# Performance work log

Measured on AMD Instinct MI355X. Metric: run time of the kernel, lower is better.

Reference implementation:

```python
import jax, jax.numpy as jnp
import numpy as np

N = 100000      # nodes
E = 1200000     # edges
F_IN = 256      # features_num
HID = 64        # hidden_dim = max(64, 2*32)
NC = 32         # num_class
H = 2           # GAT heads (edge_num < 1.4M)
GAT_SLOPE = 0.2 # GATConv internal LeakyReLU
ACT_SLOPE = 0.01  # F.leaky_relu default


def _glorot(k, shape):
    lim = float(np.sqrt(6.0 / (shape[0] + shape[-1])))
    return jax.random.uniform(k, shape, minval=-lim, maxval=lim, dtype=jnp.float32)


def setup_inputs() -> dict:
    key = jax.random.key(0)
    ks = jax.random.split(key, 32)
    inp = {
        "x": jax.random.normal(ks[0], (N, F_IN), dtype=jnp.float32),
        "edge_index": jax.random.randint(ks[1], (2, E), 0, N, dtype=jnp.int32),
        "edge_weight": jax.random.uniform(ks[2], (E,), dtype=jnp.float32),
    }
    in_dims = [F_IN, 3 * HID]  # layer2 input is cell.output_dim = HID*(1+H)
    ki = 3
    for l, d in enumerate(in_dims):
        inp[f"pre_W{l}"] = _glorot(ks[ki], (d, HID)); ki += 1
        inp[f"pre_b{l}"] = jnp.zeros((HID,), jnp.float32)
        inp[f"gat_W{l}"] = _glorot(ks[ki], (HID, H * HID)); ki += 1
        inp[f"att_src{l}"] = _glorot(ks[ki], (H, HID)); ki += 1
        inp[f"att_dst{l}"] = _glorot(ks[ki], (H, HID)); ki += 1
        inp[f"gat_b{l}"] = jnp.zeros((H * HID,), jnp.float32)
        inp[f"sg_W{l}"] = _glorot(ks[ki], (HID, HID)); ki += 1
        inp[f"sg_b{l}"] = jnp.zeros((HID,), jnp.float32)
    inp["cls_W"] = _glorot(ks[ki], (3 * HID, NC))
    inp["cls_b"] = jnp.zeros((NC,), jnp.float32)
    return inp


def _gat_conv(x, src, dst, W, att_src, att_dst, b):
    # src/dst already include self-loops. x: [N, HID]
    xp = (x @ W).reshape(N, H, HID)                       # [N, H, C]
    a_src = jnp.sum(xp * att_src, axis=-1)                # [N, H]
    a_dst = jnp.sum(xp * att_dst, axis=-1)                # [N, H]
    e = jax.nn.leaky_relu(a_src[src] + a_dst[dst], GAT_SLOPE)  # [E', H]
    m = jax.ops.segment_max(e, dst, num_segments=N)       # segment softmax over dst
    e = jnp.exp(e - m[dst])
    s = jax.ops.segment_sum(e, dst, num_segments=N)
    alpha = e / (s[dst] + 1e-16)
    out = jax.ops.segment_sum(xp[src] * alpha[:, :, None], dst, num_segments=N)
    return out.reshape(N, H * HID) + b


def _sg_conv(x, src_sl, dst_sl, w_sl, W, b):
    # gcn_norm with self-loops (weight 1) already appended; K=1 propagation then linear
    deg = jax.ops.segment_sum(w_sl, dst_sl, num_segments=N)
    dinv = jnp.where(deg > 0, jax.lax.rsqrt(deg), 0.0)
    norm = dinv[src_sl] * w_sl * dinv[dst_sl]             # [E']
    h = jax.ops.segment_sum(x[src_sl] * norm[:, None], dst_sl, num_segments=N)
    return h @ W + b


def _forward(x, edge_index, edge_weight, params):
    src, dst = edge_index[0], edge_index[1]
    loop = jnp.arange(N, dtype=src.dtype)
    src_sl = jnp.concatenate([src, loop])
    dst_sl = jnp.concatenate([dst, loop])
    w_sl = jnp.concatenate([edge_weight, jnp.ones((N,), edge_weight.dtype)])
    for l in range(2):
        pre_W, pre_b, gat_W, a_s, a_d, gat_b, sg_W, sg_b = params[l]
        xh = x @ pre_W + pre_b                            # preprocessor_x
        o1 = jax.nn.leaky_relu(_gat_conv(xh, src_sl, dst_sl, gat_W, a_s, a_d, gat_b), ACT_SLOPE)
        o2 = jax.nn.leaky_relu(_sg_conv(xh, src_sl, dst_sl, w_sl, sg_W, sg_b), ACT_SLOPE)
        x = jax.nn.relu(jnp.concatenate([o1, o2], axis=1))  # [N, 3*HID]
    cls_W, cls_b = params[2]
    logits = x @ cls_W + cls_b
    return jax.nn.log_softmax(logits, axis=-1)


def reference(x, edge_index, edge_weight,
              pre_W0, pre_b0, gat_W0, att_src0, att_dst0, gat_b0, sg_W0, sg_b0,
              pre_W1, pre_b1, gat_W1, att_src1, att_dst1, gat_b1, sg_W1, sg_b1,
              cls_W, cls_b):
    params = [
        (pre_W0, pre_b0, gat_W0, att_src0, att_dst0, gat_b0, sg_W0, sg_b0),
        (pre_W1, pre_b1, gat_W1, att_src1, att_dst1, gat_b1, sg_W1, sg_b1),
        (cls_W, cls_b),
    ]
    return _forward(x, edge_index, edge_weight, params)
```

## Files before the change

kernel.cpp:

```cpp
#include <hip/hip_runtime.h>
#include <hip/hip_fp16.h>
#include <math.h>

#define NN 100000
#define NE 1200000
#define FIN 256
#define NBLK 391
#define HB 4688

using half8   = __attribute__((ext_vector_type(8))) _Float16;
using floatx4 = __attribute__((ext_vector_type(4))) float;

__device__ __forceinline__ floatx4 mfma16(half8 a, half8 b, floatx4 c) {
    return __builtin_amdgcn_mfma_f32_16x16x32_f16(a, b, c, 0, 0, 0);
}

__global__ __launch_bounds__(256) void k_prep(const int* __restrict__ dst,
                                              const float* __restrict__ ew,
                                              unsigned long long* __restrict__ packed,
                                              int* __restrict__ ord,
                                              const float* __restrict__ W0,
                                              const float* __restrict__ W1,
                                              const float* __restrict__ Wg0,
                                              const float* __restrict__ Ws0,
                                              const float* __restrict__ Wg1,
                                              const float* __restrict__ Ws1,
                                              const float* __restrict__ Wc,
                                              const float* __restrict__ As0,
                                              const float* __restrict__ Ad0,
                                              const float* __restrict__ As1,
                                              const float* __restrict__ Ad1,
                                              __half* __restrict__ Wf,
                                              float* __restrict__ attf) {
    int bid = blockIdx.x;
    if (bid < HB) {
        int e = bid * 256 + threadIdx.x;
        if (e >= NE) return;
        int d = dst[e]; float w = ew[e];
        unsigned long long add = (1ULL << 48)
            + (unsigned long long)((double)w * 4294967296.0);
        unsigned long long old = atomicAdd(&packed[d], add);
        ord[e] = (int)(old >> 48);
        return;
    }
    int o = (bid - HB) * 256 + threadIdx.x;
    if (o >= 59904) return;
    if (o >= 59392) {
        int idx = o - 59392;
        int layer = idx >> 8, rem = idx & 255;
        int v = rem >> 6, c = rem & 63, h = v & 1;
        const float* Wg = layer ? Wg1 : Wg0;
        const float* av = (v < 2) ? (layer ? As1 : As0) : (layer ? Ad1 : Ad0);
        float s = 0.f;
        for (int jj = 0; jj < 64; ++jj)
            s = fmaf(Wg[c * 128 + h * 64 + jj], av[h * 64 + jj], s);
        attf[idx] = s;
        return;
    }
    int lo, NT, N; const float* Wg; const float* Wsg = nullptr;
    if (o < 16384)      { lo = o;         NT = 4;  N = 64; Wg = W0; }
    else if (o < 28672) { lo = o - 16384; NT = 4;  N = 64; Wg = W1; }
    else if (o < 40960) { lo = o - 28672; NT = 12; N = 0;  Wg = Wg0; Wsg = Ws0; }
    else if (o < 53248) { lo = o - 40960; NT = 12; N = 0;  Wg = Wg1; Wsg = Ws1; }
    else                { lo = o - 53248; NT = 2;  N = 32; Wg = Wc; }
    int j = lo & 7, n = (lo >> 3) & 15, q = (lo >> 7) & 3, rest = lo >> 9;
    int t = rest % NT, kc = rest / NT;
    int k = kc * 32 + q * 8 + j, col = t * 16 + n;
    float v;
    if (Wsg) v = (col < 128) ? Wg[(size_t)k * 128 + col] : Wsg[(size_t)k * 64 + (col - 128)];
    else     v = Wg[(size_t)k * N + col];
    Wf[o] = __float2half(v);
}

__global__ __launch_bounds__(256) void k_scanA(const unsigned long long* __restrict__ packed,
                                               int* __restrict__ row_ptr,
                                               int* __restrict__ bsum,
                                               float* __restrict__ asd) {
    __shared__ int tmp[256];
    int tid = threadIdx.x;
    int i = blockIdx.x * 256 + tid;
    int v = 0;
    if (i < NN) {
        unsigned long long p = packed[i];
        v = (int)(p >> 48);
        double deg = (double)(p & 0xFFFFFFFFFFFFULL) * (1.0 / 4294967296.0) + 1.0;
        asd[i * 4 + 2] = rsqrtf((float)deg);
    }
    tmp[tid] = v;
    __syncthreads();
    for (int off = 1; off < 256; off <<= 1) {
        int t = (tid >= off) ? tmp[tid - off] : 0;
        __syncthreads();
        tmp[tid] += t;
        __syncthreads();
    }
    if (i < NN) row_ptr[i] = tmp[tid] - v;
    if (tid == 255) bsum[blockIdx.x] = tmp[255];
}

__global__ __launch_bounds__(512) void k_scanB(int* __restrict__ bsum) {
    __shared__ int tmp[512];
    int tid = threadIdx.x;
    int v = (tid < NBLK) ? bsum[tid] : 0;
    tmp[tid] = v;
    __syncthreads();
    for (int off = 1; off < 512; off <<= 1) {
        int t = (tid >= off) ? tmp[tid - off] : 0;
        __syncthreads();
        tmp[tid] += t;
        __syncthreads();
    }
    if (tid < NBLK) bsum[tid] = tmp[tid] - v;
}

__global__ __launch_bounds__(256) void k_scanC(int* __restrict__ row_ptr,
                                               const int* __restrict__ bsum) {
    int i = blockIdx.x * 256 + threadIdx.x;
    if (i < NN) row_ptr[i] += bsum[i >> 8];
    if (i == 0) row_ptr[NN] = NE;
}

__global__ __launch_bounds__(256) void k_fill(const int* __restrict__ src,
                                              const int* __restrict__ dst,
                                              const float* __restrict__ ew,
                                              const int* __restrict__ row_ptr,
                                              const int* __restrict__ ord,
                                              int2* __restrict__ recs) {
    int e = blockIdx.x * 256 + threadIdx.x;
    if (e >= NE) return;
    int d = dst[e];
    int pos = row_ptr[d] + ord[e];
    int2 r; r.x = src[e]; r.y = __float_as_int(ew[e]);
    recs[pos] = r;
}

__device__ __forceinline__ void pre_epi(floatx4* acc, const float* b, const float* attf,
                                        float* asd, float* a_dst, __half* out,
                                        int rowb, int q, int n) {
    float vs0[4] = {0,0,0,0}, vs1[4] = {0,0,0,0};
    float vd0[4] = {0,0,0,0}, vd1[4] = {0,0,0,0};
    #pragma unroll
    for (int t = 0; t < 4; ++t) {
        float bb  = b[t * 16 + n];
        float ws0 = attf[t * 16 + n],       ws1 = attf[64 + t * 16 + n];
        float wd0 = attf[128 + t * 16 + n], wd1 = attf[192 + t * 16 + n];
        #pragma unroll
        for (int r = 0; r < 4; ++r) {
            float xv = acc[t][r] + bb;
            int row = rowb + q * 4 + r;
            if (row < NN) out[(size_t)row * 64 + t * 16 + n] = __float2half(xv);
            vs0[r] = fmaf(xv, ws0, vs0[r]);
            vs1[r] = fmaf(xv, ws1, vs1[r]);
            vd0[r] = fmaf(xv, wd0, vd0[r]);
            vd1[r] = fmaf(xv, wd1, vd1[r]);
        }
    }
    #pragma unroll
    for (int off = 1; off < 16; off <<= 1) {
        #pragma unroll
        for (int r = 0; r < 4; ++r) {
            vs0[r] += __shfl_xor(vs0[r], off);
            vs1[r] += __shfl_xor(vs1[r], off);
            vd0[r] += __shfl_xor(vd0[r], off);
            vd1[r] += __shfl_xor(vd1[r], off);
        }
    }
    if (n == 0) {
        #pragma unroll
        for (int r = 0; r < 4; ++r) {
            int row = rowb + q * 4 + r;
            if (row < NN) {
                *(float2*)&asd[row * 4] = make_float2(vs0[r], vs1[r]);
                *(float2*)&a_dst[row * 2] = make_float2(vd0[r], vd1[r]);
            }
        }
    }
}

template<int KK>
__global__ __launch_bounds__(256) void k_pre32(const float* __restrict__ A,
                                               const __half* __restrict__ Wf,
                                               const float* __restrict__ b,
                                               const float* __restrict__ attf,
                                               float* __restrict__ asd,
                                               float* __restrict__ a_dst,
                                               __half* __restrict__ out) {
    int lane = threadIdx.x & 63, wv = threadIdx.x >> 6;
    int q = lane >> 4, n = lane & 15;
    int rowb = blockIdx.x * 64 + wv * 16;
    int rowA = rowb + n; if (rowA > NN - 1) rowA = NN - 1;
    floatx4 acc[4] = {};
    const float* ap = A + (size_t)rowA * KK + q * 8;
    const __half* wp = Wf + q * 128 + n * 8;
    #pragma unroll
    for (int kc = 0; kc < KK / 32; ++kc) {
        float4 f0 = *(const float4*)(ap + kc * 32);
        float4 f1 = *(const float4*)(ap + kc * 32 + 4);
        half8 a;
        a[0] = (_Float16)f0.x; a[1] = (_Float16)f0.y;
        a[2] = (_Float16)f0.z; a[3] = (_Float16)f0.w;
        a[4] = (_Float16)f1.x; a[5] = (_Float16)f1.y;
        a[6] = (_Float16)f1.z; a[7] = (_Float16)f1.w;
        #pragma unroll
        for (int t = 0; t < 4; ++t) {
            half8 bf = *(const half8*)(wp + (size_t)(kc * 4 + t) * 512);
            acc[t] = mfma16(a, bf, acc[t]);
        }
    }
    pre_epi(acc, b, attf, asd, a_dst, out, rowb, q, n);
}

__global__ __launch_bounds__(256) void k_pre16(const __half* __restrict__ A,
                                               const __half* __restrict__ Wf,
                                               const float* __restrict__ b,
                                               const float* __restrict__ attf,
                                               float* __restrict__ asd,
                                               float* __restrict__ a_dst,
                                               __half* __restrict__ out) {
    int lane = threadIdx.x & 63, wv = threadIdx.x >> 6;
    int q = lane >> 4, n = lane & 15;
    int rowb = blockIdx.x * 64 + wv * 16;
    int rowA = rowb + n; if (rowA > NN - 1) rowA = NN - 1;
    floatx4 acc[4] = {};
    const __half* ap = A + (size_t)rowA * 192 + q * 8;
    const __half* wp = Wf + q * 128 + n * 8;
    #pragma unroll
    for (int kc = 0; kc < 6; ++kc) {
        half8 a = *(const half8*)(ap + kc * 32);
        #pragma unroll
        for (int t = 0; t < 4; ++t) {
            half8 bf = *(const half8*)(wp + (size_t)(kc * 4 + t) * 512);
            acc[t] = mfma16(a, bf, acc[t]);
        }
    }
    pre_epi(acc, b, attf, asd, a_dst, out, rowb, q, n);
}

__global__ __launch_bounds__(256) void k_post(const __half* __restrict__ A,
                                              const __half* __restrict__ Wf,
                                              const float* __restrict__ gat_b,
                                              const float* __restrict__ sg_b,
                                              __half* __restrict__ out) {
    int lane = threadIdx.x & 63, wv = threadIdx.x >> 6;
    int q = lane >> 4, n = lane & 15;
    int rowb = blockIdx.x * 64 + wv * 16;
    int rowA = rowb + n; if (rowA > NN - 1) rowA = NN - 1;
    floatx4 acc[12] = {};
    const __half* ap = A + (size_t)rowA * 192 + q * 8;
    const __half* wp = Wf + q * 128 + n * 8;
    #pragma unroll
    for (int g = 0; g < 3; ++g) {
        #pragma unroll
        for (int kc = 0; kc < 2; ++kc) {
            half8 a = *(const half8*)(ap + g * 64 + kc * 32);
            #pragma unroll
            for (int tt = 0; tt < 4; ++tt) {
                int t = g * 4 + tt;
                half8 bf = *(const half8*)(wp + (size_t)(kc * 12 + t) * 512);
                acc[t] = mfma16(a, bf, acc[t]);
            }
        }
    }
    #pragma unroll
    for (int t = 0; t < 12; ++t) {
        float bb = (t < 8) ? gat_b[t * 16 + n] : sg_b[(t - 8) * 16 + n];
        #pragma unroll
        for (int r = 0; r < 4; ++r) {
            int row = rowb + q * 4 + r;
            if (row < NN)
                out[(size_t)row * 192 + t * 16 + n] =
                    __float2half(fmaxf(acc[t][r] + bb, 0.f));
        }
    }
}

__global__ __launch_bounds__(256) void k_clsm(const __half* __restrict__ A,
                                              const __half* __restrict__ Wf,
                                              const float* __restrict__ b,
                                              float* __restrict__ out) {
    int lane = threadIdx.x & 63, wv = threadIdx.x >> 6;
    int q = lane >> 4, n = lane & 15;
    int rowb = blockIdx.x * 64 + wv * 16;
    int rowA = rowb + n; if (rowA > NN - 1) rowA = NN - 1;
    floatx4 acc[2] = {};
    const __half* ap = A + (size_t)rowA * 192 + q * 8;
    const __half* wp = Wf + q * 128 + n * 8;
    #pragma unroll
    for (int kc = 0; kc < 6; ++kc) {
        half8 a = *(const half8*)(ap + kc * 32);
        #pragma unroll
        for (int t = 0; t < 2; ++t) {
            half8 bf = *(const half8*)(wp + (size_t)(kc * 2 + t) * 512);
            acc[t] = mfma16(a, bf, acc[t]);
        }
    }
    float b0 = b[n], b1 = b[16 + n];
    #pragma unroll
    for (int r = 0; r < 4; ++r) {
        float v0 = acc[0][r] + b0, v1 = acc[1][r] + b1;
        float mx = fmaxf(v0, v1);
        #pragma unroll
        for (int off = 1; off < 16; off <<= 1) mx = fmaxf(mx, __shfl_xor(mx, off));
        float sm = __expf(v0 - mx) + __expf(v1 - mx);
        #pragma unroll
        for (int off = 1; off < 16; off <<= 1) sm += __shfl_xor(sm, off);
        float lg = mx + __logf(sm);
        int row = rowb + q * 4 + r;
        if (row < NN) {
            out[(size_t)row * 32 + n]      = v0 - lg;
            out[(size_t)row * 32 + 16 + n] = v1 - lg;
        }
    }
}

__global__ __launch_bounds__(256) void k_agg(const int* __restrict__ row_ptr,
                                             const int2* __restrict__ recs,
                                             const float* __restrict__ asd,
                                             const float* __restrict__ a_dst,
                                             const __half* __restrict__ xh,
                                             __half* __restrict__ agg) {
    __shared__ float4 einfo[4][64];
    int lane = threadIdx.x & 63;
    int wv = threadIdx.x >> 6;
    int d = blockIdx.x * 4 + wv;
    if (d >= NN) return;
    int p0 = row_ptr[d], p1 = row_ptr[d + 1];
    int nn = p1 - p0;
    float2 ad2 = ((const float2*)a_dst)[d];
    const float4* asd4 = (const float4*)asd;
    int sub = lane >> 5;
    unsigned flb = (unsigned)(lane & 31) * 4u;

    float g00 = 0.f, g01 = 0.f;
    float g10 = 0.f, g11 = 0.f;
    float s0a = 0.f, s1a = 0.f;

#define EDGE_ACC(E) do {                                                        \
        unsigned off_ = (unsigned)__float_as_int((E).w) + flb;                  \
        float2 v_ = __half22float2(*(const __half2*)((const char*)xh + off_));  \
        g00 = fmaf((E).x, v_.x, g00); g01 = fmaf((E).x, v_.y, g01);             \
        g10 = fmaf((E).y, v_.x, g10); g11 = fmaf((E).y, v_.y, g11);             \
        s0a = fmaf((E).z, v_.x, s0a); s1a = fmaf((E).z, v_.y, s1a);             \
    } while (0)

    if (nn <= 63) {
        int tot = nn + 1;
        float v0 = -INFINITY, v1 = -INFINITY, ewq = 0.f; int es = 0;
        if (lane < tot) {
            float wraw;
            if (lane < nn) {
                int2 rec = recs[p0 + lane];
                es = rec.x;
                wraw = __int_as_float(rec.y);
            } else { es = d; wraw = 1.f; }
            float4 a4 = asd4[es];
            v0 = a4.x + ad2.x; v0 = (v0 > 0.f) ? v0 : 0.2f * v0;
            v1 = a4.y + ad2.y; v1 = (v1 > 0.f) ? v1 : 0.2f * v1;
            ewq = wraw * a4.z;
        }
        float m0 = v0, m1 = v1;
        #pragma unroll
        for (int off = 32; off; off >>= 1) {
            m0 = fmaxf(m0, __shfl_xor(m0, off));
            m1 = fmaxf(m1, __shfl_xor(m1, off));
        }
        float e0 = (lane < tot) ? __expf(v0 - m0) : 0.f;
        float e1 = (lane < tot) ? __expf(v1 - m1) : 0.f;
        float s0 = e0, s1 = e1;
        #pragma unroll
        for (int off = 32; off; off >>= 1) {
            s0 += __shfl_xor(s0, off);
            s1 += __shfl_xor(s1, off);
        }
        if (lane < tot)
            einfo[wv][lane] = make_float4(e0 / (s0 + 1e-16f), e1 / (s1 + 1e-16f),
                                          ewq, __int_as_float(es << 7));
        const float4* ep = &einfo[wv][sub];
        int j = 0;
        for (; j + 4 <= tot; j += 4) {
            float4 eA = ep[j];
            float4 eB = ep[j + 2];
            EDGE_ACC(eA);
            EDGE_ACC(eB);
        }
        for (; j + 2 <= tot; j += 2) {
            float4 eA = ep[j];
            EDGE_ACC(eA);
        }
        if (tot & 1) {
            if (sub == 0) {
                float4 eT = einfo[wv][tot - 1];
                EDGE_ACC(eT);
            }
        }
    } else {
        float4 aself = asd4[d];
        float sv0 = aself.x + ad2.x; sv0 = (sv0 > 0.f) ? sv0 : 0.2f * sv0;
        float sv1 = aself.y + ad2.y; sv1 = (sv1 > 0.f) ? sv1 : 0.2f * sv1;
        float m0 = sv0, m1 = sv1;
        for (int e = p0 + lane; e < p1; e += 64) {
            int s = recs[e].x;
            float4 a4 = asd4[s];
            float v0 = a4.x + ad2.x; v0 = (v0 > 0.f) ? v0 : 0.2f * v0;
            float v1 = a4.y + ad2.y; v1 = (v1 > 0.f) ? v1 : 0.2f * v1;
            m0 = fmaxf(m0, v0); m1 = fmaxf(m1, v1);
        }
        #pragma unroll
        for (int off = 32; off; off >>= 1) {
            m0 = fmaxf(m0, __shfl_xor(m0, off));
            m1 = fmaxf(m1, __shfl_xor(m1, off));
        }
        float s0 = 0.f, s1 = 0.f;
        for (int e = p0 + lane; e < p1; e += 64) {
            int s = recs[e].x;
            float4 a4 = asd4[s];
            float v0 = a4.x + ad2.x; v0 = (v0 > 0.f) ? v0 : 0.2f * v0;
            float v1 = a4.y + ad2.y; v1 = (v1 > 0.f) ? v1 : 0.2f * v1;
            s0 += __expf(v0 - m0); s1 += __expf(v1 - m1);
        }
        #pragma unroll
        for (int off = 32; off; off >>= 1) {
            s0 += __shfl_xor(s0, off);
            s1 += __shfl_xor(s1, off);
        }
        s0 += __expf(sv0 - m0); s1 += __expf(sv1 - m1);
        float inv0 = 1.f / (s0 + 1e-16f), inv1 = 1.f / (s1 + 1e-16f);
        for (int base = p0; base < p1; base += 64) {
            int e = base + lane;
            int nc = min(64, p1 - base);
            if (e < p1) {
                int2 rec = recs[e];
                int es = rec.x;
                float4 a4 = asd4[es];
                float v0 = a4.x + ad2.x; v0 = (v0 > 0.f) ? v0 : 0.2f * v0;
                float v1 = a4.y + ad2.y; v1 = (v1 > 0.f) ? v1 : 0.2f * v1;
                einfo[wv][lane] = make_float4(__expf(v0 - m0) * inv0,
                                              __expf(v1 - m1) * inv1,
                                              __int_as_float(rec.y) * a4.z,
                                              __int_as_float(es << 7));
            }
            const float4* ep = &einfo[wv][sub];
            int j = 0;
            for (; j + 2 <= nc; j += 2) {
                float4 eA = ep[j];
                EDGE_ACC(eA);
            }
            if (nc & 1) {
                if (sub == 0) {
                    float4 eT = einfo[wv][nc - 1];
                    EDGE_ACC(eT);
                }
            }
        }
        if (sub == 0) {
            float4 eS = make_float4(__expf(sv0 - m0) * inv0,
                                    __expf(sv1 - m1) * inv1,
                                    aself.z, __int_as_float(d << 7));
            EDGE_ACC(eS);
        }
    }
#undef EDGE_ACC

    g00 += __shfl_xor(g00, 32); g01 += __shfl_xor(g01, 32);
    g10 += __shfl_xor(g10, 32); g11 += __shfl_xor(g11, 32);
    s0a += __shfl_xor(s0a, 32); s1a += __shfl_xor(s1a, 32);

    float did = asd[d * 4 + 2];
    __half* op = agg + (size_t)d * 192;
    int fp = (lane & 31) * 2;
    if (lane < 32) {
        *(__half2*)(op + fp)       = __floats2half2_rn(g00, g01);
        *(__half2*)(op + 128 + fp) = __floats2half2_rn(s0a * did, s1a * did);
    } else {
        *(__half2*)(op + 64 + fp)  = __floats2half2_rn(g10, g11);
    }
}

extern "C" void kernel_launch(void* const* d_in, const int* in_sizes, int n_in,
                              void* d_out, int out_size, void* d_ws, size_t ws_size,
                              hipStream_t stream) {
    const float* x   = (const float*)d_in[0];
    const int*   ei  = (const int*)d_in[1];
    const float* ew  = (const float*)d_in[2];
    const int* src = ei;
    const int* dst = ei + NE;

    const float* P[2][8];
    for (int l = 0; l < 2; ++l)
        for (int j = 0; j < 8; ++j)
            P[l][j] = (const float*)d_in[3 + l * 8 + j];
    const float* cls_W = (const float*)d_in[19];
    const float* cls_b = (const float*)d_in[20];

    float* ws = (float*)d_ws;
    const size_t n = NN;
    __half* xh_h = (__half*)(ws);
    __half* agg  = (__half*)(ws + 32 * n);
    float* asd   = ws + 128 * n;
    float* a_dst = ws + 132 * n;
    __half* xA_h = (__half*)(ws + 134 * n);
    __half* xB_h = (__half*)(ws + 230 * n);
    __half* Wf   = (__half*)(ws + 326 * n);
    float* attf  = ws + 326 * n + 29696;
    float* base2 = ws + 326 * n + 30208;
    unsigned long long* packed = (unsigned long long*)base2;
    int*   row_ptr    = (int*)(packed + NN);
    int*   bsum       = row_ptr + (NN + 1);
    int*   ord        = bsum + 513;
    int2*  recs       = (int2*)(ord + NE);

    __half* Wf_pre0 = Wf;
    __half* Wf_pre1 = Wf + 16384;
    __half* Wf_pq0  = Wf + 28672;
    __half* Wf_pq1  = Wf + 40960;
    __half* Wf_cls  = Wf + 53248;

    const int TB = 256;
    int gb_edge  = (NE + TB - 1) / TB;
    int gb_node  = (NN + TB - 1) / TB;
    int gb_wave4 = (NN + 3) / 4;
    int gb64     = (NN + 63) / 64;

    hipMemsetAsync(packed, 0, NN * sizeof(unsigned long long), stream);
    k_prep<<<HB + (59904 + TB - 1) / TB, TB, 0, stream>>>(
        dst, ew, packed, ord,
        P[0][0], P[1][0], P[0][2], P[0][6], P[1][2], P[1][6], cls_W,
        P[0][3], P[0][4], P[1][3], P[1][4], Wf, attf);

    k_scanA<<<NBLK, TB, 0, stream>>>(packed, row_ptr, bsum, asd);
    k_scanB<<<1, 512, 0, stream>>>(bsum);
    k_scanC<<<gb_node, TB, 0, stream>>>(row_ptr, bsum);
    k_fill <<<gb_edge, TB, 0, stream>>>(src, dst, ew, row_ptr, ord, recs);

    for (int l = 0; l < 2; ++l) {
        const float* pre_b = P[l][1];
        const float* gat_b = P[l][5];
        const float* sg_b  = P[l][7];
        __half* xout = (l == 0) ? xA_h : xB_h;

        if (l == 0)
            k_pre32<256><<<gb64, TB, 0, stream>>>(x, Wf_pre0, pre_b,
                                                  attf, asd, a_dst, xh_h);
        else
            k_pre16<<<gb64, TB, 0, stream>>>(xA_h, Wf_pre1, pre_b,
                                             attf + 256, asd, a_dst, xh_h);
        k_agg <<<gb_wave4, TB, 0, stream>>>(row_ptr, recs, asd, a_dst, xh_h, agg);
        k_post<<<gb64, TB, 0, stream>>>(agg, (l == 0) ? Wf_pq0 : Wf_pq1,
                                        gat_b, sg_b, xout);
    }

    k_clsm<<<gb64, TB, 0, stream>>>(xB_h, Wf_cls, cls_b, (float*)d_out);
}
```

Before: 501.9 us.

## Fuse layer-0 preprocess into prep, single-pass decoupled scan, fuse post with next GEMM

Moves the layer-0 input projection into the prep kernel, where it runs in extra blocks alongside the degree-counting atomics. Replaces the three-kernel scan with a single-pass decoupled-lookback scan. Fuses each post-GEMM with the following pre-GEMM or classifier through a shared-memory tile, so the intermediate xA/xB activations never go to global memory. This cuts launches and HBM round trips, but the lookback relies on inter-block spin-waiting and the fused kernels use more shared memory.

```diff
diff --git a/kernel.cpp b/kernel.cpp
--- a/kernel.cpp
+++ b/kernel.cpp
@@ -7,18 +7,64 @@
 #define FIN 256
 #define NBLK 391
 #define HB 4688
+#define WB 170
+#define GB64 1563
 
 using half8   = __attribute__((ext_vector_type(8))) _Float16;
 using floatx4 = __attribute__((ext_vector_type(4))) float;
 
 __device__ __forceinline__ floatx4 mfma16(half8 a, half8 b, floatx4 c) {
     return __builtin_amdgcn_mfma_f32_16x16x32_f16(a, b, c, 0, 0, 0);
+}
+
+__device__ __forceinline__ void pre_epi(floatx4* acc, const float* b, const float* attf,
+                                        float* asd, float* a_dst, __half* out,
+                                        int rowb, int q, int n) {
+    float vs0[4] = {0,0,0,0}, vs1[4] = {0,0,0,0};
+    float vd0[4] = {0,0,0,0}, vd1[4] = {0,0,0,0};
+    #pragma unroll
+    for (int t = 0; t < 4; ++t) {
+        float bb  = b[t * 16 + n];
+        float ws0 = attf[t * 16 + n],       ws1 = attf[64 + t * 16 + n];
+        float wd0 = attf[128 + t * 16 + n], wd1 = attf[192 + t * 16 + n];
+        #pragma unroll
+        for (int r = 0; r < 4; ++r) {
+            float xv = acc[t][r] + bb;
+            int row = rowb + q * 4 + r;
+            if (row < NN) out[(size_t)row * 64 + t * 16 + n] = __float2half(xv);
+            vs0[r] = fmaf(xv, ws0, vs0[r]);
+            vs1[r] = fmaf(xv, ws1, vs1[r]);
+            vd0[r] = fmaf(xv, wd0, vd0[r]);
+            vd1[r] = fmaf(xv, wd1, vd1[r]);
+        }
+    }
+    #pragma unroll
+    for (int off = 1; off < 16; off <<= 1) {
+        #pragma unroll
+        for (int r = 0; r < 4; ++r) {
+            vs0[r] += __shfl_xor(vs0[r], off);
+            vs1[r] += __shfl_xor(vs1[r], off);
+            vd0[r] += __shfl_xor(vd0[r], off);
+            vd1[r] += __shfl_xor(vd1[r], off);
+        }
+    }
+    if (n == 0) {
+        #pragma unroll
+        for (int r = 0; r < 4; ++r) {
+            int row = rowb + q * 4 + r;
+            if (row < NN) {
+                *(float2*)&asd[row * 4] = make_float2(vs0[r], vs1[r]);
+                *(float2*)&a_dst[row * 2] = make_float2(vd0[r], vd1[r]);
+            }
+        }
+    }
 }
 
 __global__ __launch_bounds__(256) void k_prep(const int* __restrict__ dst,
                                               const float* __restrict__ ew,
                                               unsigned long long* __restrict__ packed,
                                               int* __restrict__ ord,
+                                              const float* __restrict__ x,
                                               const float* __restrict__ W0,
                                               const float* __restrict__ W1,
                                               const float* __restrict__ Wg0,
@@ -30,11 +76,18 @@
                                               const float* __restrict__ Ad0,
                                               const float* __restrict__ As1,
                                               const float* __restrict__ Ad1,
+                                              const float* __restrict__ pre_b0,
                                               __half* __restrict__ Wf,
-                                              float* __restrict__ attf) {
+                                              float* __restrict__ attf,
+                                              float* __restrict__ asd,
+                                              float* __restrict__ a_dst,
+                                              __half* __restrict__ xh) {
+    __shared__ __half Wl[16384];
+    __shared__ float attL[256];
     int bid = blockIdx.x;
+    int tid = threadIdx.x;
     if (bid < HB) {
-        int e = bid * 256 + threadIdx.x;
+        int e = bid * 256 + tid;
         if (e >= NE) return;
         int d = dst[e]; float w = ew[e];
         unsigned long long add = (1ULL << 48)
@@ -43,42 +96,84 @@
         ord[e] = (int)(old >> 48);
         return;
     }
-    int o = (bid - HB) * 256 + threadIdx.x;
-    if (o >= 59904) return;
-    if (o >= 59392) {
-        int idx = o - 59392;
-        int layer = idx >> 8, rem = idx & 255;
-        int v = rem >> 6, c = rem & 63, h = v & 1;
-        const float* Wg = layer ? Wg1 : Wg0;
-        const float* av = (v < 2) ? (layer ? As1 : As0) : (layer ? Ad1 : Ad0);
+    if (bid < HB + WB) {
+        int o = (bid - HB) * 256 + tid + 16384;
+        if (o >= 59904) return;
+        if (o >= 59392) {
+            int idx = o - 59392;
+            int layer = idx >> 8, rem = idx & 255;
+            int v = rem >> 6, c = rem & 63, h = v & 1;
+            const float* Wg = layer ? Wg1 : Wg0;
+            const float* av = (v < 2) ? (layer ? As1 : As0) : (layer ? Ad1 : Ad0);
+            float s = 0.f;
+            for (int jj = 0; jj < 64; ++jj)
+                s = fmaf(Wg[c * 128 + h * 64 + jj], av[h * 64 + jj], s);
+            attf[idx] = s;
+            return;
+        }
+        int lo, NT, N; const float* Wg; const float* Wsg = nullptr;
+        if (o < 28672)      { lo = o - 16384; NT = 4;  N = 64; Wg = W1; }
+        else if (o < 40960) { lo = o - 28672; NT = 12; N = 0;  Wg = Wg0; Wsg = Ws0; }
+        else if (o < 53248) { lo = o - 40960; NT = 12; N = 0;  Wg = Wg1; Wsg = Ws1; }
+        else                { lo = o - 53248; NT = 2;  N = 32; Wg = Wc; }
+        int j = lo & 7, n = (lo >> 3) & 15, q = (lo >> 7) & 3, rest = lo >> 9;
+        int t = rest % NT, kc = rest / NT;
+        int k = kc * 32 + q * 8 + j, col = t * 16 + n;
+        float v;
+        if (Wsg) v = (col < 128) ? Wg[(size_t)k * 128 + col] : Wsg[(size_t)k * 64 + (col - 128)];
+        else     v = Wg[(size_t)k * N + col];
+        Wf[o] = __float2half(v);
+        return;
+    }
+    int pb = bid - (HB + WB);
+    for (int i = tid; i < 16384; i += 256) {
+        int j = i & 7, n = (i >> 3) & 15, q = (i >> 7) & 3, rest = i >> 9;
+        int t = rest & 3, kc = rest >> 2;
+        int k = kc * 32 + q * 8 + j, col = t * 16 + n;
+        Wl[i] = __float2half(W0[(size_t)k * 64 + col]);
+    }
+    {
+        int v = tid >> 6, c = tid & 63, h = v & 1;
+        const float* av = (v < 2) ? As0 : Ad0;
         float s = 0.f;
         for (int jj = 0; jj < 64; ++jj)
-            s = fmaf(Wg[c * 128 + h * 64 + jj], av[h * 64 + jj], s);
-        attf[idx] = s;
-        return;
-    }
-    int lo, NT, N; const float* Wg; const float* Wsg = nullptr;
-    if (o < 16384)      { lo = o;         NT = 4;  N = 64; Wg = W0; }
-    else if (o < 28672) { lo = o - 16384; NT = 4;  N = 64; Wg = W1; }
-    else if (o < 40960) { lo = o - 28672; NT = 12; N = 0;  Wg = Wg0; Wsg = Ws0; }
-    else if (o < 53248) { lo = o - 40960; NT = 12; N = 0;  Wg = Wg1; Wsg = Ws1; }
-    else                { lo = o - 53248; NT = 2;  N = 32; Wg = Wc; }
-    int j = lo & 7, n = (lo >> 3) & 15, q = (lo >> 7) & 3, rest = lo >> 9;
-    int t = rest % NT, kc = rest / NT;
-    int k = kc * 32 + q * 8 + j, col = t * 16 + n;
-    float v;
-    if (Wsg) v = (col < 128) ? Wg[(size_t)k * 128 + col] : Wsg[(size_t)k * 64 + (col - 128)];
-    else     v = Wg[(size_t)k * N + col];
-    Wf[o] = __float2half(v);
-}
-
-__global__ __launch_bounds__(256) void k_scanA(const unsigned long long* __restrict__ packed,
-                                               int* __restrict__ row_ptr,
-                                               int* __restrict__ bsum,
-                                               float* __restrict__ asd) {
+            s = fmaf(Wg0[c * 128 + h * 64 + jj], av[h * 64 + jj], s);
+        attL[tid] = s;
+    }
+    __syncthreads();
+    int lane = tid & 63, wvv = tid >> 6;
+    int q = lane >> 4, n = lane & 15;
+    int rowb = pb * 64 + wvv * 16;
+    int rowA = rowb + n; if (rowA > NN - 1) rowA = NN - 1;
+    floatx4 acc[4] = {};
+    const float* ap = x + (size_t)rowA * FIN + q * 8;
+    const __half* wp = Wl + q * 128 + n * 8;
+    #pragma unroll
+    for (int kc = 0; kc < FIN / 32; ++kc) {
+        float4 f0 = *(const float4*)(ap + kc * 32);
+        float4 f1 = *(const float4*)(ap + kc * 32 + 4);
+        half8 a;
+        a[0] = (_Float16)f0.x; a[1] = (_Float16)f0.y;
+        a[2] = (_Float16)f0.z; a[3] = (_Float16)f0.w;
+        a[4] = (_Float16)f1.x; a[5] = (_Float16)f1.y;
+        a[6] = (_Float16)f1.z; a[7] = (_Float16)f1.w;
+        #pragma unroll
+        for (int t = 0; t < 4; ++t) {
+            half8 bf = *(const half8*)(wp + (size_t)(kc * 4 + t) * 512);
+            acc[t] = mfma16(a, bf, acc[t]);
+        }
+    }
+    pre_epi(acc, pre_b0, attL, asd, a_dst, xh, rowb, q, n);
+}
+
+__global__ __launch_bounds__(256) void k_scan(const unsigned long long* __restrict__ packed,
+                                              int* __restrict__ row_ptr,
+                                              float* __restrict__ asd,
+                                              unsigned long long* __restrict__ desc) {
     __shared__ int tmp[256];
-    int tid = threadIdx.x;
-    int i = blockIdx.x * 256 + tid;
+    __shared__ int exoff_sh;
+    int tid = threadIdx.x, bid = blockIdx.x;
+    int i = bid * 256 + tid;
     int v = 0;
     if (i < NN) {
         unsigned long long p = packed[i];
@@ -94,30 +189,45 @@
         tmp[tid] += t;
         __syncthreads();
     }
-    if (i < NN) row_ptr[i] = tmp[tid] - v;
-    if (tid == 255) bsum[blockIdx.x] = tmp[255];
-}
-
-__global__ __launch_bounds__(512) void k_scanB(int* __restrict__ bsum) {
-    __shared__ int tmp[512];
-    int tid = threadIdx.x;
-    int v = (tid < NBLK) ? bsum[tid] : 0;
-    tmp[tid] = v;
+    int bsum = tmp[255];
+    if (bid == 0) {
+        if (tid == 0) {
+            exoff_sh = 0;
+            atomicExch(&desc[0], (2ULL << 32) | (unsigned long long)(unsigned)bsum);
+            row_ptr[NN] = NE;
+        }
+    } else if (tid < 64) {
+        if (tid == 0)
+            atomicExch(&desc[bid], (1ULL << 32) | (unsigned long long)(unsigned)bsum);
+        int sum = 0;
+        int base = bid - 1;
+        for (;;) {
+            int j = base - tid;
+            unsigned long long d = 0;
+            bool have = (j >= 0);
+            if (have) {
+                do { d = atomicAdd((unsigned long long*)&desc[j], 0ULL); }
+                while ((d >> 32) == 0ULL);
+            }
+            unsigned long long m2 = __ballot(have && ((d >> 32) == 2ULL));
+            if (m2) {
+                int stop = __ffsll((long long)m2) - 1;
+                if (tid <= stop) sum += (int)(d & 0xFFFFFFFFULL);
+                break;
+            }
+            if (have) sum += (int)(d & 0xFFFFFFFFULL);
+            base -= 64;
+        }
+        #pragma unroll
+        for (int off = 32; off; off >>= 1) sum += __shfl_xor(sum, off);
+        if (tid == 0) {
+            exoff_sh = sum;
+            atomicExch(&desc[bid],
+                       (2ULL << 32) | (unsigned long long)(unsigned)(sum + bsum));
+        }
+    }
     __syncthreads();
-    for (int off = 1; off < 512; off <<= 1) {
-        int t = (tid >= off) ? tmp[tid - off] : 0;
-        __syncthreads();
-        tmp[tid] += t;
-        __syncthreads();
-    }
-    if (tid < NBLK) bsum[tid] = tmp[tid] - v;
-}
-
-__global__ __launch_bounds__(256) void k_scanC(int* __restrict__ row_ptr,
-                                               const int* __restrict__ bsum) {
-    int i = blockIdx.x * 256 + threadIdx.x;
-    if (i < NN) row_ptr[i] += bsum[i >> 8];
-    if (i == 0) row_ptr[NN] = NE;
+    if (i < NN) row_ptr[i] = exoff_sh + tmp[tid] - v;
 }
 
 __global__ __launch_bounds__(256) void k_fill(const int* __restrict__ src,
@@ -132,185 +242,6 @@
     int pos = row_ptr[d] + ord[e];
     int2 r; r.x = src[e]; r.y = __float_as_int(ew[e]);
     recs[pos] = r;
-}
-
-__device__ __forceinline__ void pre_epi(floatx4* acc, const float* b, const float* attf,
-                                        float* asd, float* a_dst, __half* out,
-                                        int rowb, int q, int n) {
-    float vs0[4] = {0,0,0,0}, vs1[4] = {0,0,0,0};
-    float vd0[4] = {0,0,0,0}, vd1[4] = {0,0,0,0};
-    #pragma unroll
-    for (int t = 0; t < 4; ++t) {
-        float bb  = b[t * 16 + n];
-        float ws0 = attf[t * 16 + n],       ws1 = attf[64 + t * 16 + n];
-        float wd0 = attf[128 + t * 16 + n], wd1 = attf[192 + t * 16 + n];
-        #pragma unroll
-        for (int r = 0; r < 4; ++r) {
-            float xv = acc[t][r] + bb;
-            int row = rowb + q * 4 + r;
-            if (row < NN) out[(size_t)row * 64 + t * 16 + n] = __float2half(xv);
-            vs0[r] = fmaf(xv, ws0, vs0[r]);
-            vs1[r] = fmaf(xv, ws1, vs1[r]);
-            vd0[r] = fmaf(xv, wd0, vd0[r]);
-            vd1[r] = fmaf(xv, wd1, vd1[r]);
-        }
-    }
-    #pragma unroll
-    for (int off = 1; off < 16; off <<= 1) {
-        #pragma unroll
-        for (int r = 0; r < 4; ++r) {
-            vs0[r] += __shfl_xor(vs0[r], off);
-            vs1[r] += __shfl_xor(vs1[r], off);
-            vd0[r] += __shfl_xor(vd0[r], off);
-            vd1[r] += __shfl_xor(vd1[r], off);
-        }
-    }
-    if (n == 0) {
-        #pragma unroll
-        for (int r = 0; r < 4; ++r) {
-            int row = rowb + q * 4 + r;
-            if (row < NN) {
-                *(float2*)&asd[row * 4] = make_float2(vs0[r], vs1[r]);
-                *(float2*)&a_dst[row * 2] = make_float2(vd0[r], vd1[r]);
-            }
-        }
-    }
-}
-
-template<int KK>
-__global__ __launch_bounds__(256) void k_pre32(const float* __restrict__ A,
-                                               const __half* __restrict__ Wf,
-                                               const float* __restrict__ b,
-                                               const float* __restrict__ attf,
-                                               float* __restrict__ asd,
-                                               float* __restrict__ a_dst,
-                                               __half* __restrict__ out) {
-    int lane = threadIdx.x & 63, wv = threadIdx.x >> 6;
-    int q = lane >> 4, n = lane & 15;
-    int rowb = blockIdx.x * 64 + wv * 16;
-    int rowA = rowb + n; if (rowA > NN - 1) rowA = NN - 1;
-    floatx4 acc[4] = {};
-    const float* ap = A + (size_t)rowA * KK + q * 8;
-    const __half* wp = Wf + q * 128 + n * 8;
-    #pragma unroll
-    for (int kc = 0; kc < KK / 32; ++kc) {
-        float4 f0 = *(const float4*)(ap + kc * 32);
-        float4 f1 = *(const float4*)(ap + kc * 32 + 4);
-        half8 a;
-        a[0] = (_Float16)f0.x; a[1] = (_Float16)f0.y;
-        a[2] = (_Float16)f0.z; a[3] = (_Float16)f0.w;
-        a[4] = (_Float16)f1.x; a[5] = (_Float16)f1.y;
-        a[6] = (_Float16)f1.z; a[7] = (_Float16)f1.w;
-        #pragma unroll
-        for (int t = 0; t < 4; ++t) {
-            half8 bf = *(const half8*)(wp + (size_t)(kc * 4 + t) * 512);
-            acc[t] = mfma16(a, bf, acc[t]);
-        }
-    }
-    pre_epi(acc, b, attf, asd, a_dst, out, rowb, q, n);
-}
-
-__global__ __launch_bounds__(256) void k_pre16(const __half* __restrict__ A,
-                                               const __half* __restrict__ Wf,
-                                               const float* __restrict__ b,
-                                               const float* __restrict__ attf,
-                                               float* __restrict__ asd,
-                                               float* __restrict__ a_dst,
-                                               __half* __restrict__ out) {
-    int lane = threadIdx.x & 63, wv = threadIdx.x >> 6;
-    int q = lane >> 4, n = lane & 15;
-    int rowb = blockIdx.x * 64 + wv * 16;
-    int rowA = rowb + n; if (rowA > NN - 1) rowA = NN - 1;
-    floatx4 acc[4] = {};
-    const __half* ap = A + (size_t)rowA * 192 + q * 8;
-    const __half* wp = Wf + q * 128 + n * 8;
-    #pragma unroll
-    for (int kc = 0; kc < 6; ++kc) {
-        half8 a = *(const half8*)(ap + kc * 32);
-        #pragma unroll
-        for (int t = 0; t < 4; ++t) {
-            half8 bf = *(const half8*)(wp + (size_t)(kc * 4 + t) * 512);
-            acc[t] = mfma16(a, bf, acc[t]);
-        }
-    }
-    pre_epi(acc, b, attf, asd, a_dst, out, rowb, q, n);
-}
-
-__global__ __launch_bounds__(256) void k_post(const __half* __restrict__ A,
-                                              const __half* __restrict__ Wf,
-                                              const float* __restrict__ gat_b,
-                                              const float* __restrict__ sg_b,
-                                              __half* __restrict__ out) {
-    int lane = threadIdx.x & 63, wv = threadIdx.x >> 6;
-    int q = lane >> 4, n = lane & 15;
-    int rowb = blockIdx.x * 64 + wv * 16;
-    int rowA = rowb + n; if (rowA > NN - 1) rowA = NN - 1;
-    floatx4 acc[12] = {};
-    const __half* ap = A + (size_t)rowA * 192 + q * 8;
-    const __half* wp = Wf + q * 128 + n * 8;
-    #pragma unroll
-    for (int g = 0; g < 3; ++g) {
-        #pragma unroll
-        for (int kc = 0; kc < 2; ++kc) {
-            half8 a = *(const half8*)(ap + g * 64 + kc * 32);
-            #pragma unroll
-            for (int tt = 0; tt < 4; ++tt) {
-                int t = g * 4 + tt;
-                half8 bf = *(const half8*)(wp + (size_t)(kc * 12 + t) * 512);
-                acc[t] = mfma16(a, bf, acc[t]);
-            }
-        }
-    }
-    #pragma unroll
-    for (int t = 0; t < 12; ++t) {
-        float bb = (t < 8) ? gat_b[t * 16 + n] : sg_b[(t - 8) * 16 + n];
-        #pragma unroll
-        for (int r = 0; r < 4; ++r) {
-            int row = rowb + q * 4 + r;
-            if (row < NN)
-                out[(size_t)row * 192 + t * 16 + n] =
-                    __float2half(fmaxf(acc[t][r] + bb, 0.f));
-        }
-    }
-}
-
-__global__ __launch_bounds__(256) void k_clsm(const __half* __restrict__ A,
-                                              const __half* __restrict__ Wf,
-                                              const float* __restrict__ b,
-                                              float* __restrict__ out) {
-    int lane = threadIdx.x & 63, wv = threadIdx.x >> 6;
-    int q = lane >> 4, n = lane & 15;
-    int rowb = blockIdx.x * 64 + wv * 16;
-    int rowA = rowb + n; if (rowA > NN - 1) rowA = NN - 1;
-    floatx4 acc[2] = {};
-    const __half* ap = A + (size_t)rowA * 192 + q * 8;
-    const __half* wp = Wf + q * 128 + n * 8;
-    #pragma unroll
-    for (int kc = 0; kc < 6; ++kc) {
-        half8 a = *(const half8*)(ap + kc * 32);
-        #pragma unroll
-        for (int t = 0; t < 2; ++t) {
-            half8 bf = *(const half8*)(wp + (size_t)(kc * 2 + t) * 512);
-            acc[t] = mfma16(a, bf, acc[t]);
-        }
-    }
-    float b0 = b[n], b1 = b[16 + n];
-    #pragma unroll
-    for (int r = 0; r < 4; ++r) {
-        float v0 = acc[0][r] + b0, v1 = acc[1][r] + b1;
-        float mx = fmaxf(v0, v1);
-        #pragma unroll
-        for (int off = 1; off < 16; off <<= 1) mx = fmaxf(mx, __shfl_xor(mx, off));
-        float sm = __expf(v0 - mx) + __expf(v1 - mx);
-        #pragma unroll
-        for (int off = 1; off < 16; off <<= 1) sm += __shfl_xor(sm, off);
-        float lg = mx + __logf(sm);
-        int row = rowb + q * 4 + r;
-        if (row < NN) {
-            out[(size_t)row * 32 + n]      = v0 - lg;
-            out[(size_t)row * 32 + 16 + n] = v1 - lg;
-        }
-    }
 }
 
 __global__ __launch_bounds__(256) void k_agg(const int* __restrict__ row_ptr,
@@ -476,6 +407,143 @@
     }
 }
 
+__global__ __launch_bounds__(256) void k_postpre(const __half* __restrict__ A,
+                                                 const __half* __restrict__ Wfpq,
+                                                 const float* __restrict__ gat_b,
+                                                 const float* __restrict__ sg_b,
+                                                 const __half* __restrict__ Wfpre,
+                                                 const float* __restrict__ pre_b,
+                                                 const float* __restrict__ attf,
+                                                 float* __restrict__ asd,
+                                                 float* __restrict__ a_dst,
+                                                 __half* __restrict__ xh) {
+    __shared__ __half tile[64][200];
+    int lane = threadIdx.x & 63, wv = threadIdx.x >> 6;
+    int q = lane >> 4, n = lane & 15;
+    int rowb = blockIdx.x * 64 + wv * 16;
+    int rowA = rowb + n; if (rowA > NN - 1) rowA = NN - 1;
+    {
+        floatx4 acc[12] = {};
+        const __half* ap = A + (size_t)rowA * 192 + q * 8;
+        const __half* wp = Wfpq + q * 128 + n * 8;
+        #pragma unroll
+        for (int g = 0; g < 3; ++g) {
+            #pragma unroll
+            for (int kc = 0; kc < 2; ++kc) {
+                half8 a = *(const half8*)(ap + g * 64 + kc * 32);
+                #pragma unroll
+                for (int tt = 0; tt < 4; ++tt) {
+                    int t = g * 4 + tt;
+                    half8 bf = *(const half8*)(wp + (size_t)(kc * 12 + t) * 512);
+                    acc[t] = mfma16(a, bf, acc[t]);
+                }
+            }
+        }
+        #pragma unroll
+        for (int t = 0; t < 12; ++t) {
+            float bb = (t < 8) ? gat_b[t * 16 + n] : sg_b[(t - 8) * 16 + n];
+            #pragma unroll
+            for (int r = 0; r < 4; ++r) {
+                int row = rowb + q * 4 + r;
+                float v = fmaxf(acc[t][r] + bb, 0.f);
+                tile[wv * 16 + q * 4 + r][t * 16 + n] =
+                    (row < NN) ? __float2half(v) : __half(0.f);
+            }
+        }
+    }
+    __syncthreads();
+    {
+        floatx4 acc[4] = {};
+        const __half* ap2 = &tile[wv * 16 + n][q * 8];
+        const __half* wp = Wfpre + q * 128 + n * 8;
+        #pragma unroll
+        for (int kc = 0; kc < 6; ++kc) {
+            half8 a = *(const half8*)(ap2 + kc * 32);
+            #pragma unroll
+            for (int t = 0; t < 4; ++t) {
+                half8 bf = *(const half8*)(wp + (size_t)(kc * 4 + t) * 512);
+                acc[t] = mfma16(a, bf, acc[t]);
+            }
+        }
+        pre_epi(acc, pre_b, attf, asd, a_dst, xh, rowb, q, n);
+    }
+}
+
+__global__ __launch_bounds__(256) void k_postcls(const __half* __restrict__ A,
+                                                 const __half* __restrict__ Wfpq,
+                                                 const float* __restrict__ gat_b,
+                                                 const float* __restrict__ sg_b,
+                                                 const __half* __restrict__ Wfcls,
+                                                 const float* __restrict__ b,
+                                                 float* __restrict__ out) {
+    __shared__ __half tile[64][200];
+    int lane = threadIdx.x & 63, wv = threadIdx.x >> 6;
+    int q = lane >> 4, n = lane & 15;
+    int rowb = blockIdx.x * 64 + wv * 16;
+    int rowA = rowb + n; if (rowA > NN - 1) rowA = NN - 1;
+    {
+        floatx4 acc[12] = {};
+        const __half* ap = A + (size_t)rowA * 192 + q * 8;
+        const __half* wp = Wfpq + q * 128 + n * 8;
+        #pragma unroll
+        for (int g = 0; g < 3; ++g) {
+            #pragma unroll
+            for (int kc = 0; kc < 2; ++kc) {
+                half8 a = *(const half8*)(ap + g * 64 + kc * 32);
+                #pragma unroll
+                for (int tt = 0; tt < 4; ++tt) {
+                    int t = g * 4 + tt;
+                    half8 bf = *(const half8*)(wp + (size_t)(kc * 12 + t) * 512);
+                    acc[t] = mfma16(a, bf, acc[t]);
+                }
+            }
+        }
+        #pragma unroll
+        for (int t = 0; t < 12; ++t) {
+            float bb = (t < 8) ? gat_b[t * 16 + n] : sg_b[(t - 8) * 16 + n];
+            #pragma unroll
+            for (int r = 0; r < 4; ++r) {
+                int row = rowb + q * 4 + r;
+                float v = fmaxf(acc[t][r] + bb, 0.f);
+                tile[wv * 16 + q * 4 + r][t * 16 + n] =
+                    (row < NN) ? __float2half(v) : __half(0.f);
+            }
+        }
+    }
+    __syncthreads();
+    {
+        floatx4 acc[2] = {};
+        const __half* ap2 = &tile[wv * 16 + n][q * 8];
+        const __half* wp = Wfcls + q * 128 + n * 8;
+        #pragma unroll
+        for (int kc = 0; kc < 6; ++kc) {
+            half8 a = *(const half8*)(ap2 + kc * 32);
+            #pragma unroll
+            for (int t = 0; t < 2; ++t) {
+                half8 bf = *(const half8*)(wp + (size_t)(kc * 2 + t) * 512);
+                acc[t] = mfma16(a, bf, acc[t]);
+            }
+        }
+        float b0 = b[n], b1 = b[16 + n];
+        #pragma unroll
+        for (int r = 0; r < 4; ++r) {
+            float v0 = acc[0][r] + b0, v1 = acc[1][r] + b1;
+            float mx = fmaxf(v0, v1);
+            #pragma unroll
+            for (int off = 1; off < 16; off <<= 1) mx = fmaxf(mx, __shfl_xor(mx, off));
+            float sm = __expf(v0 - mx) + __expf(v1 - mx);
+            #pragma unroll
+            for (int off = 1; off < 16; off <<= 1) sm += __shfl_xor(sm, off);
+            float lg = mx + __logf(sm);
+            int row = rowb + q * 4 + r;
+            if (row < NN) {
+                out[(size_t)row * 32 + n]      = v0 - lg;
+                out[(size_t)row * 32 + 16 + n] = v1 - lg;
+            }
+        }
+    }
+}
+
 extern "C" void kernel_launch(void* const* d_in, const int* in_sizes, int n_in,
                               void* d_out, int out_size, void* d_ws, size_t ws_size,
                               hipStream_t stream) {
@@ -498,18 +566,15 @@
     __half* agg  = (__half*)(ws + 32 * n);
     float* asd   = ws + 128 * n;
     float* a_dst = ws + 132 * n;
-    __half* xA_h = (__half*)(ws + 134 * n);
-    __half* xB_h = (__half*)(ws + 230 * n);
-    __half* Wf   = (__half*)(ws + 326 * n);
-    float* attf  = ws + 326 * n + 29696;
-    float* base2 = ws + 326 * n + 30208;
+    __half* Wf   = (__half*)(ws + 134 * n);
+    float* attf  = ws + 134 * n + 29696;
+    float* base2 = ws + 134 * n + 30208;
     unsigned long long* packed = (unsigned long long*)base2;
-    int*   row_ptr    = (int*)(packed + NN);
-    int*   bsum       = row_ptr + (NN + 1);
-    int*   ord        = bsum + 513;
+    unsigned long long* desc   = packed + NN;
+    int*   row_ptr    = (int*)(desc + NBLK);
+    int*   ord        = row_ptr + (NN + 2);
     int2*  recs       = (int2*)(ord + NE);
 
-    __half* Wf_pre0 = Wf;
     __half* Wf_pre1 = Wf + 16384;
     __half* Wf_pq0  = Wf + 28672;
     __half* Wf_pq1  = Wf + 40960;
@@ -517,37 +582,23 @@
 
     const int TB = 256;
     int gb_edge  = (NE + TB - 1) / TB;
-    int gb_node  = (NN + TB - 1) / TB;
     int gb_wave4 = (NN + 3) / 4;
-    int gb64     = (NN + 63) / 64;
-
-    hipMemsetAsync(packed, 0, NN * sizeof(unsigned long long), stream);
-    k_prep<<<HB + (59904 + TB - 1) / TB, TB, 0, stream>>>(
-        dst, ew, packed, ord,
+
+    hipMemsetAsync(packed, 0, (NN + NBLK) * sizeof(unsigned long long), stream);
+    k_prep<<<HB + WB + GB64, TB, 0, stream>>>(
+        dst, ew, packed, ord, x,
         P[0][0], P[1][0], P[0][2], P[0][6], P[1][2], P[1][6], cls_W,
-        P[0][3], P[0][4], P[1][3], P[1][4], Wf, attf);
-
-    k_scanA<<<NBLK, TB, 0, stream>>>(packed, row_ptr, bsum, asd);
-    k_scanB<<<1, 512, 0, stream>>>(bsum);
-    k_scanC<<<gb_node, TB, 0, stream>>>(row_ptr, bsum);
-    k_fill <<<gb_edge, TB, 0, stream>>>(src, dst, ew, row_ptr, ord, recs);
-
-    for (int l = 0; l < 2; ++l) {
-        const float* pre_b = P[l][1];
-        const float* gat_b = P[l][5];
-        const float* sg_b  = P[l][7];
-        __half* xout = (l == 0) ? xA_h : xB_h;
-
-        if (l == 0)
-            k_pre32<256><<<gb64, TB, 0, stream>>>(x, Wf_pre0, pre_b,
-                                                  attf, asd, a_dst, xh_h);
-        else
-            k_pre16<<<gb64, TB, 0, stream>>>(xA_h, Wf_pre1, pre_b,
-                                             attf + 256, asd, a_dst, xh_h);
-        k_agg <<<gb_wave4, TB, 0, stream>>>(row_ptr, recs, asd, a_dst, xh_h, agg);
-        k_post<<<gb64, TB, 0, stream>>>(agg, (l == 0) ? Wf_pq0 : Wf_pq1,
-                                        gat_b, sg_b, xout);
-    }
-
-    k_clsm<<<gb64, TB, 0, stream>>>(xB_h, Wf_cls, cls_b, (float*)d_out);
-}
+        P[0][3], P[0][4], P[1][3], P[1][4], P[0][1],
+        Wf, attf, asd, a_dst, xh_h);
+
+    k_scan<<<NBLK, TB, 0, stream>>>(packed, row_ptr, asd, desc);
+    k_fill<<<gb_edge, TB, 0, stream>>>(src, dst, ew, row_ptr, ord, recs);
+
+    k_agg    <<<gb_wave4, TB, 0, stream>>>(row_ptr, recs, asd, a_dst, xh_h, agg);
+    k_postpre<<<GB64, TB, 0, stream>>>(agg, Wf_pq0, P[0][5], P[0][7],
+                                       Wf_pre1, P[1][1], attf + 256,
+                                       asd, a_dst, xh_h);
+    k_agg    <<<gb_wave4, TB, 0, stream>>>(row_ptr, recs, asd, a_dst, xh_h, agg);
+    k_postcls<<<GB64, TB, 0, stream>>>(agg, Wf_pq1, P[1][5], P[1][7],
+                                       Wf_cls, cls_b, (float*)d_out);
+}
```

Result: faster. 482.7 us (-3.8%).
